# Optimization experiments

Hardware: AMD Instinct MI355X
Metric: run time of the kernel (lower is better)

## Reference

```python
import jax, jax.numpy as jnp
import numpy as np

TEMP = 0.3
K_ANCHORS = 512
SK_ITERS = 4  # max_iter=4 in the original; tol early-exit omitted (fixed small iter count)
EPS = 1e-12   # F.normalize clamp_min eps


def setup_inputs() -> dict:
    key = jax.random.key(0)
    k1, k2 = jax.random.split(key)
    x = jax.random.normal(k1, (16, 256, 64, 64), dtype=jnp.float32)
    some_idx = jax.random.randint(k2, (K_ANCHORS,), 0, 64 * 64, dtype=jnp.int32)
    return {"x": x, "some_idx": some_idx}


def sinkhorn_knopp(A):
    # A: [M, k], strictly positive. Normalize by total mass, then alternate
    # L1 column / row normalization (p=1 normalize on positive entries == sum-divide).
    A = A / A.sum()
    def body(A, _):
        A = A / jnp.clip(A.sum(axis=0, keepdims=True), EPS)  # columns
        A = A / jnp.clip(A.sum(axis=1, keepdims=True), EPS)  # rows
        return A, None
    A, _ = jax.lax.scan(body, A, None, length=SK_ITERS)
    return A


def reference(x, some_idx):
    N, C, H, W = x.shape
    k = some_idx.shape[0]
    # L2-normalize over channel dim (F.normalize dim=1)
    l2_x = x / jnp.clip(jnp.linalg.norm(x, axis=1, keepdims=True), EPS)
    # gather k random spatial anchors -> [N, C, k]
    some_x = jnp.take(l2_x.reshape(N, C, H * W), some_idx, axis=-1)
    # cosine scores [N, k, H, W]
    scores = jnp.einsum('nchw,nck->nkhw', l2_x, some_x)
    # flatten to [N*H*W, k], exponentiate, Sinkhorn-Knopp
    A = jnp.exp(scores.transpose(0, 2, 3, 1).reshape(-1, k) / TEMP)
    A = sinkhorn_knopp(A)
    Kmat = A.reshape(N, H, W, k).transpose(0, 3, 1, 2)  # [N, k, H, W]
    # reconstruct from anchors
    return jnp.einsum('nkhw,nck->nchw', Kmat, some_x)
```

## Files before the change

kernel.cpp:

```cpp
#include <hip/hip_runtime.h>
#include <hip/hip_bf16.h>
#include <hip/hip_fp16.h>
#include <hip/hip_fp8.h>

#define N_B 16
#define C_DIM 256
#define HW 4096
#define M_TOT (N_B*HW)
#define K_A 512
#define TEMP_INV (1.0f/0.3f)
#define EPS_SK 1e-12f

typedef _Float16 f16x8 __attribute__((ext_vector_type(8)));
typedef _Float16 f16x4 __attribute__((ext_vector_type(4)));
typedef float f32x4 __attribute__((ext_vector_type(4)));
typedef float f32x2 __attribute__((ext_vector_type(2)));

#if defined(__has_builtin)
#if __has_builtin(__builtin_amdgcn_cvt_pk_fp8_f32) && __has_builtin(__builtin_amdgcn_cvt_pk_f32_fp8)
#define HW_FP8 1
#endif
#endif

__device__ __forceinline__ int vperm(int j){
    return (j & ~63) | ((j & 15) << 2) | ((j & 63) >> 4);
}
__device__ __forceinline__ int ivp(int s){
    return (s & ~63) | ((s & 3) << 4) | ((s & 63) >> 2);
}

#define GLOBAL_AS __attribute__((address_space(1)))
#define LDS_AS __attribute__((address_space(3)))
__device__ __forceinline__ void gload_lds16(const void* g, void* l){
    __builtin_amdgcn_global_load_lds((GLOBAL_AS const void*)g, (LDS_AS void*)l, 16, 0, 0);
}

__device__ __forceinline__ f16x8 fp8x8_to_f16x8(uint2 a){
    f16x8 h;
#ifdef HW_FP8
    f32x2 q0 = __builtin_amdgcn_cvt_pk_f32_fp8((int)a.x, false);
    f32x2 q1 = __builtin_amdgcn_cvt_pk_f32_fp8((int)a.x, true);
    f32x2 q2 = __builtin_amdgcn_cvt_pk_f32_fp8((int)a.y, false);
    f32x2 q3 = __builtin_amdgcn_cvt_pk_f32_fp8((int)a.y, true);
    h[0]=(_Float16)q0[0]; h[1]=(_Float16)q0[1]; h[2]=(_Float16)q1[0]; h[3]=(_Float16)q1[1];
    h[4]=(_Float16)q2[0]; h[5]=(_Float16)q2[1]; h[6]=(_Float16)q3[0]; h[7]=(_Float16)q3[1];
#else
    union { uint2 u; __hip_fp8_e4m3 b8[8]; } cv; cv.u = a;
    #pragma unroll
    for (int e = 0; e < 8; ++e) h[e] = (_Float16)(float)cv.b8[e];
#endif
    return h;
}

__global__ __launch_bounds__(256) void k_normtrans(const float* __restrict__ x,
                                                   _Float16* __restrict__ Lt,
                                                   float* __restrict__ v){
    __shared__ float tl[32][257];
    __shared__ float red[8][32];
    __shared__ float invs[32];
    int n   = blockIdx.x >> 7;
    int hw0 = (blockIdx.x & 127) * 32;
    if (blockIdx.x < 2) v[blockIdx.x*256 + threadIdx.x] = 1.0f;
    int tx4 = threadIdx.x & 7;
    int cy  = threadIdx.x >> 3;
    const float* px = x + ((size_t)(n*C_DIM + cy))*HW + hw0 + tx4*4;
    #pragma unroll
    for (int r = 0; r < 8; ++r){
        float4 xv = *(const float4*)(px + (size_t)(r*32)*HW);
        int c = cy + r*32;
        tl[tx4*4+0][c] = xv.x;
        tl[tx4*4+1][c] = xv.y;
        tl[tx4*4+2][c] = xv.z;
        tl[tx4*4+3][c] = xv.w;
    }
    __syncthreads();
    int tx = threadIdx.x & 31, ty = threadIdx.x >> 5;
    float ss = 0.f;
    #pragma unroll
    for (int cc = 0; cc < 32; ++cc){
        float tv = tl[tx][cc*8 + ty];
        ss += tv*tv;
    }
    red[ty][tx] = ss;
    __syncthreads();
    if (ty == 0){
        float s = red[0][tx]+red[1][tx]+red[2][tx]+red[3][tx]
                + red[4][tx]+red[5][tx]+red[6][tx]+red[7][tx];
        invs[tx] = 1.0f / fmaxf(sqrtf(s), 1e-12f);
    }
    __syncthreads();
    #pragma unroll
    for (int r = 0; r < 4; ++r){
        int hwl = ty + r*8;
        float inv = invs[hwl];
        f16x8 h;
        #pragma unroll
        for (int e = 0; e < 8; ++e) h[e] = (_Float16)(tl[hwl][tx*8 + e] * inv);
        *(f16x8*)&Lt[((size_t)(n*HW + hw0 + hwl))*C_DIM + tx*8] = h;
    }
}

__global__ __launch_bounds__(256) void k_gather(const _Float16* __restrict__ Lt,
                                                const int* __restrict__ sidx,
                                                _Float16* __restrict__ sxT){
    int n  = blockIdx.y;
    int jj = blockIdx.x*8 + (threadIdx.x >> 5);
    int c8 = (threadIdx.x & 31) * 8;
    int p  = sidx[jj];
    *(f16x8*)&sxT[((size_t)(n*K_A + jj))*C_DIM + c8] =
        *(const f16x8*)&Lt[((size_t)(n*HW + p))*C_DIM + c8];
}

__global__ __launch_bounds__(256) void k_gemm1(const _Float16* __restrict__ Lt,
                                               const _Float16* __restrict__ sxT,
                                               unsigned* __restrict__ A8,
                                               float* __restrict__ part){
    __shared__ _Float16 As[3*128*32];
    __shared__ _Float16 Bs[3*128*32];
    __shared__ float colred[4][128];
    const int swz = (blockIdx.x & 7)*256 + (blockIdx.x >> 3);
    const int jb = swz & 3, mb = (swz >> 2) & 31, nb = swz >> 7;
    const int mbase = mb * 128;
    const int jbase = jb * 128;
    const int t = threadIdx.x;
    const int lane = t & 63, w = t >> 6;
    const int wm = (w >> 1)*64, wn = (w & 1)*64;
    const int l15 = lane & 15, lq = lane >> 4;

    f32x4 acc[4][4] = {};
    const _Float16* pa = Lt  + ((size_t)(nb*HW  + mbase))*C_DIM;
    const _Float16* pb = sxT + ((size_t)(nb*K_A + jbase))*C_DIM;

    const int r0 = t >> 2, ch = t & 3;
    const int r1 = r0 + 64;
    const int cs0 = (ch ^ ((r0 >> 1) & 3)) << 3;
    const int cs1 = (ch ^ ((r1 >> 1) & 3)) << 3;

#define STAGE1(buf, kt) { int k0 = (kt)*32; \
    gload_lds16(pa + (size_t)r0*C_DIM + k0 + cs0, &As[(buf)*4096 + t*8]); \
    gload_lds16(pa + (size_t)r1*C_DIM + k0 + cs1, &As[(buf)*4096 + (256+t)*8]); \
    gload_lds16(pb + (size_t)r0*C_DIM + k0 + cs0, &Bs[(buf)*4096 + t*8]); \
    gload_lds16(pb + (size_t)r1*C_DIM + k0 + cs1, &Bs[(buf)*4096 + (256+t)*8]); }

    STAGE1(0, 0); STAGE1(1, 1);
    #pragma unroll
    for (int kt = 0; kt < 8; ++kt){
        __builtin_amdgcn_s_barrier();
        __builtin_amdgcn_sched_barrier(0);
        if (kt < 6) STAGE1((kt+2)%3, kt+2);
        if (kt < 6)      asm volatile("s_waitcnt vmcnt(8)" ::: "memory");
        else if (kt < 7) asm volatile("s_waitcnt vmcnt(4)" ::: "memory");
        else             asm volatile("s_waitcnt vmcnt(0)" ::: "memory");
        __builtin_amdgcn_sched_barrier(0);
        const int cur = kt % 3;
        f16x8 af[4], bf[4];
        #pragma unroll
        for (int mi = 0; mi < 4; ++mi){
            int r = wm + mi*16 + l15;
            af[mi] = *(const f16x8*)&As[cur*4096 + r*32 + ((lq ^ ((r>>1)&3)) << 3)];
        }
        #pragma unroll
        for (int ni = 0; ni < 4; ++ni){
            int r = wn + ni*16 + l15;
            bf[ni] = *(const f16x8*)&Bs[cur*4096 + r*32 + ((lq ^ ((r>>1)&3)) << 3)];
        }
        #pragma unroll
        for (int mi = 0; mi < 4; ++mi)
            #pragma unroll
            for (int ni = 0; ni < 4; ++ni)
                acc[mi][ni] = __builtin_amdgcn_mfma_f32_16x16x32_f16(af[mi], bf[ni], acc[mi][ni], 0, 0, 0);
    }
    float csum[4] = {0.f, 0.f, 0.f, 0.f};
    #pragma unroll
    for (int mi = 0; mi < 4; ++mi)
        #pragma unroll
        for (int r = 0; r < 4; ++r){
            int hw = mbase + wm + mi*16 + lq*4 + r;
            float e[4];
            #pragma unroll
            for (int ni = 0; ni < 4; ++ni){
                e[ni] = __expf(acc[mi][ni][r] * TEMP_INV);
                csum[ni] += e[ni];
            }
            unsigned pk;
#ifdef HW_FP8
            pk = (unsigned)__builtin_amdgcn_cvt_pk_fp8_f32(e[0], e[1], 0, false);
            pk = (unsigned)__builtin_amdgcn_cvt_pk_fp8_f32(e[2], e[3], (int)pk, true);
#else
            union { unsigned u; __hip_fp8_e4m3 b[4]; } cv;
            cv.b[0] = __hip_fp8_e4m3(e[0]); cv.b[1] = __hip_fp8_e4m3(e[1]);
            cv.b[2] = __hip_fp8_e4m3(e[2]); cv.b[3] = __hip_fp8_e4m3(e[3]);
            pk = cv.u;
#endif
            A8[((size_t)(nb*HW + hw))*(K_A/4) + (jbase + wn)/4 + l15] = pk;
        }
    #pragma unroll
    for (int ni = 0; ni < 4; ++ni){
        float cv = csum[ni];
        cv += __shfl_xor(cv, 16);
        cv += __shfl_xor(cv, 32);
        if (lane < 16) colred[w][wn + ni*16 + l15] = cv;
    }
    __syncthreads();
    if (t < 128){
        int jj = t;
        float s = (jj < 64) ? (colred[0][jj] + colred[2][jj])
                            : (colred[1][jj] + colred[3][jj]);
        part[((size_t)(nb*32 + mb))*K_A + jbase + vperm(jj)] = s;
    }
}

__global__ __launch_bounds__(64) void k_colfinish(const float* __restrict__ part,
                                                  float* __restrict__ v, int nchunks){
    int j = blockIdx.x;
    int lane = threadIdx.x;
    float s = 0.f;
    for (int r = lane; r < nchunks; r += 64) s += part[(size_t)r*K_A + j];
    #pragma unroll
    for (int off = 32; off; off >>= 1) s += __shfl_xor(s, off);
    if (lane == 0){
        float vo = v[j];
        v[j] = 128.0f * vo / fmaxf(vo * s, EPS_SK);
    }
}

__global__ __launch_bounds__(256) void k_fused8(const unsigned* __restrict__ A8,
                                                const float* __restrict__ v,
                                                float* __restrict__ part){
    __shared__ float red[4][512];
    int b = blockIdx.x;
    int tg = threadIdx.x >> 6, lane = threadIdx.x & 63;
    float vr[8];
    const float* pv = v + (lane << 3);
    #pragma unroll
    for (int e = 0; e < 8; ++e) vr[e] = pv[e];
    float acc[8] = {};
    for (int it = 0; it < 16; ++it){
        int i = (b << 6) + (it << 2) + tg;
        uint2 a = *(const uint2*)&A8[(size_t)i*(K_A/4) + (lane << 1)];
        float av[8];
#ifdef HW_FP8
        f32x2 p0 = __builtin_amdgcn_cvt_pk_f32_fp8((int)a.x, false);
        f32x2 p1 = __builtin_amdgcn_cvt_pk_f32_fp8((int)a.x, true);
        f32x2 p2 = __builtin_amdgcn_cvt_pk_f32_fp8((int)a.y, false);
        f32x2 p3 = __builtin_amdgcn_cvt_pk_f32_fp8((int)a.y, true);
        av[0]=p0[0]; av[1]=p0[1]; av[2]=p1[0]; av[3]=p1[1];
        av[4]=p2[0]; av[5]=p2[1]; av[6]=p3[0]; av[7]=p3[1];
#else
        union { uint2 u; __hip_fp8_e4m3 b8[8]; } cv; cv.u = a;
        #pragma unroll
        for (int e = 0; e < 8; ++e) av[e] = (float)cv.b8[e];
#endif
        float r = 0.f;
        #pragma unroll
        for (int e = 0; e < 8; ++e) r += av[e] * vr[e];
        #pragma unroll
        for (int off = 32; off; off >>= 1) r += __shfl_xor(r, off);
        float un = 1.0f / fmaxf(r, EPS_SK);
        #pragma unroll
        for (int e = 0; e < 8; ++e) acc[e] += av[e] * un;
    }
    #pragma unroll
    for (int e = 0; e < 8; ++e) red[tg][(lane<<3)+e] = acc[e];
    __syncthreads();
    if (tg == 0){
        #pragma unroll
        for (int e = 0; e < 8; ++e){
            int j = (lane<<3)+e;
            part[((size_t)b)*K_A + j] = red[0][j]+red[1][j]+red[2][j]+red[3][j];
        }
    }
}

__global__ __launch_bounds__(256) void k_sxvT(const _Float16* __restrict__ sxT,
                                              const float* __restrict__ v,
                                              _Float16* __restrict__ SXv){
    __shared__ float tl[64][65];
    int n  = blockIdx.z;
    int j0 = blockIdx.x * 64;
    int c0 = blockIdx.y * 64;
    int tx = threadIdx.x & 63, ty = threadIdx.x >> 6;
    #pragma unroll
    for (int r = 0; r < 16; ++r){
        int jl = ty + r*4;
        tl[jl][tx] = (float)sxT[((size_t)(n*K_A + j0 + jl))*C_DIM + c0 + tx]
                   * v[j0 + vperm(jl)];
    }
    __syncthreads();
    #pragma unroll
    for (int r = 0; r < 16; ++r){
        int cl = ty + r*4;
        SXv[((size_t)(n*C_DIM + c0 + cl))*K_A + j0 + tx] = (_Float16)tl[ivp(tx) & 63][cl];
    }
}

__global__ __launch_bounds__(256) void k_gemm2(const _Float16* __restrict__ SXv,
                                               const unsigned* __restrict__ A8,
                                               const float* __restrict__ v,
                                               float* __restrict__ out){
    __shared__ _Float16 As[3*128*32];
    __shared__ unsigned char Bs8[3*128*32];
    __shared__ _Float16 vsh[512];
    const int swz = (blockIdx.x & 7)*128 + (blockIdx.x >> 3);
    const int mb = swz & 1, nbi = (swz >> 1) & 31, nb = swz >> 6;
    const int mbase = mb * 128;
    const int nbase = nbi * 128;
    const int t = threadIdx.x;
    const int lane = t & 63, w = t >> 6;
    const int wm = (w >> 1)*64, wn = (w & 1)*64;
    const int l15 = lane & 15, lq = lane >> 4;

    vsh[t]       = (_Float16)v[t];
    vsh[t + 256] = (_Float16)v[t + 256];

    f32x4 acc[4][4] = {};
    f32x4 racc[4] = {};
    const _Float16* pa = SXv + ((size_t)(nb*C_DIM + mbase))*K_A;
    const unsigned char* pb8 = (const unsigned char*)(A8 + ((size_t)(nb*HW + nbase))*(K_A/4));

    const int r0 = t >> 2, ch = t & 3;
    const int r1 = r0 + 64;
    const int cs0 = (ch ^ ((r0 >> 1) & 3)) << 3;
    const int cs1 = (ch ^ ((r1 >> 1) & 3)) << 3;
    const int br = t >> 1, bh = (t & 1) * 16;

#define STAGE2(buf, kt) { int k0 = (kt)*32; \
    gload_lds16(pa + (size_t)r0*K_A + k0 + cs0, &As[(buf)*4096 + t*8]); \
    gload_lds16(pa + (size_t)r1*K_A + k0 + cs1, &As[(buf)*4096 + (256+t)*8]); \
    gload_lds16(pb8 + (size_t)br*K_A + k0 + bh, &Bs8[(buf)*4096 + br*32 + bh]); }

    STAGE2(0, 0); STAGE2(1, 1);
    #pragma unroll
    for (int kt = 0; kt < 16; ++kt){
        __builtin_amdgcn_s_barrier();
        __builtin_amdgcn_sched_barrier(0);
        if (kt < 14) STAGE2((kt+2)%3, kt+2);
        if (kt < 14)      asm volatile("s_waitcnt vmcnt(6)" ::: "memory");
        else if (kt < 15) asm volatile("s_waitcnt vmcnt(3)" ::: "memory");
        else              asm volatile("s_waitcnt vmcnt(0)" ::: "memory");
        __builtin_amdgcn_sched_barrier(0);
        const int cur = kt % 3;
        f16x8 af[4], bf[4], vf;
        vf = *(const f16x8*)&vsh[kt*32 + lq*8];
        #pragma unroll
        for (int mi = 0; mi < 4; ++mi){
            int r = wm + mi*16 + l15;
            af[mi] = *(const f16x8*)&As[cur*4096 + r*32 + ((lq ^ ((r>>1)&3)) << 3)];
        }
        #pragma unroll
        for (int ni = 0; ni < 4; ++ni){
            int r = wn + ni*16 + l15;
            uint2 b8 = *(const uint2*)&Bs8[cur*4096 + r*32 + lq*8];
            bf[ni] = fp8x8_to_f16x8(b8);
        }
        #pragma unroll
        for (int mi = 0; mi < 4; ++mi)
            #pragma unroll
            for (int ni = 0; ni < 4; ++ni)
                acc[mi][ni] = __builtin_amdgcn_mfma_f32_16x16x32_f16(af[mi], bf[ni], acc[mi][ni], 0, 0, 0);
        #pragma unroll
        for (int ni = 0; ni < 4; ++ni)
            racc[ni] = __builtin_amdgcn_mfma_f32_16x16x32_f16(vf, bf[ni], racc[ni], 0, 0, 0);
    }
    float un[4];
    #pragma unroll
    for (int ni = 0; ni < 4; ++ni)
        un[ni] = 1.0f / fmaxf(racc[ni][0], EPS_SK);
    #pragma unroll
    for (int mi = 0; mi < 4; ++mi)
        #pragma unroll
        for (int ni = 0; ni < 4; ++ni)
            #pragma unroll
            for (int r = 0; r < 4; ++r){
                int c  = mbase + wm + mi*16 + lq*4 + r;
                int hw = nbase + wn + ni*16 + l15;
                out[((size_t)(nb*C_DIM + c))*HW + hw] = acc[mi][ni][r] * un[ni];
            }
}

extern "C" void kernel_launch(void* const* d_in, const int* in_sizes, int n_in,
                              void* d_out, int out_size, void* d_ws, size_t ws_size,
                              hipStream_t stream){
    const float* x  = (const float*)d_in[0];
    const int* sidx = (const int*)d_in[1];
    float* out = (float*)d_out;

    char* ws = (char*)d_ws;
    _Float16* Lt  = (_Float16*)ws;   ws += (size_t)N_B*HW*C_DIM*2;
    unsigned* A8  = (unsigned*)ws;   ws += (size_t)M_TOT*K_A;
    _Float16* sxT = (_Float16*)ws;   ws += (size_t)N_B*K_A*C_DIM*2;
    _Float16* SXv = (_Float16*)ws;   ws += (size_t)N_B*C_DIM*K_A*2;
    float*    v   = (float*)ws;      ws += (size_t)K_A*4;
    float*    part= (float*)ws;      ws += (size_t)1024*K_A*4;

    k_normtrans<<<2048, 256, 0, stream>>>(x, Lt, v);
    k_gather   <<<dim3(64,16), 256, 0, stream>>>(Lt, sidx, sxT);
    k_gemm1    <<<2048, 256, 0, stream>>>(Lt, sxT, A8, part);

    k_colfinish<<<512, 64, 0, stream>>>(part, v, 512);
    for (int it = 0; it < 3; ++it){
        k_fused8   <<<1024, 256, 0, stream>>>(A8, v, part);
        k_colfinish<<<512, 64, 0, stream>>>(part, v, 1024);
    }

    k_sxvT <<<dim3(8,4,16), 256, 0, stream>>>(sxT, v, SXv);
    k_gemm2<<<1024, 256, 0, stream>>>(SXv, A8, v, out);
}
```

Baseline: 142.9 us.

## Fold anchor gather into GEMMs and replace column-reduction kernels with atomics

Drops the separate gather kernel. gemm1 and sxvT now read anchor rows straight from the normalized tensor through sidx. Each Sinkhorn pass now atomically adds its column sums into a small per-iteration buffer instead of writing partials for a separate finish kernel, and consumers derive the scale as 128/S on the fly. This removes five kernel launches and the partial-sum traffic, and fused8 now runs with half as many blocks, each doing twice the rows. In exchange the float atomics make the sums non-deterministic, and there may be some atomic contention on 512 addresses.

```diff
diff --git a/kernel.cpp b/kernel.cpp
--- a/kernel.cpp
+++ b/kernel.cpp
@@ -54,13 +54,16 @@
 
 __global__ __launch_bounds__(256) void k_normtrans(const float* __restrict__ x,
                                                    _Float16* __restrict__ Lt,
-                                                   float* __restrict__ v){
+                                                   float* __restrict__ S){
     __shared__ float tl[32][257];
     __shared__ float red[8][32];
     __shared__ float invs[32];
     int n   = blockIdx.x >> 7;
     int hw0 = (blockIdx.x & 127) * 32;
-    if (blockIdx.x < 2) v[blockIdx.x*256 + threadIdx.x] = 1.0f;
+    if (blockIdx.x == 0){
+        #pragma unroll
+        for (int q = 0; q < 8; ++q) S[threadIdx.x + q*256] = 0.0f;
+    }
     int tx4 = threadIdx.x & 7;
     int cy  = threadIdx.x >> 3;
     const float* px = x + ((size_t)(n*C_DIM + cy))*HW + hw0 + tx4*4;
@@ -100,21 +103,10 @@
     }
 }
 
-__global__ __launch_bounds__(256) void k_gather(const _Float16* __restrict__ Lt,
-                                                const int* __restrict__ sidx,
-                                                _Float16* __restrict__ sxT){
-    int n  = blockIdx.y;
-    int jj = blockIdx.x*8 + (threadIdx.x >> 5);
-    int c8 = (threadIdx.x & 31) * 8;
-    int p  = sidx[jj];
-    *(f16x8*)&sxT[((size_t)(n*K_A + jj))*C_DIM + c8] =
-        *(const f16x8*)&Lt[((size_t)(n*HW + p))*C_DIM + c8];
-}
-
 __global__ __launch_bounds__(256) void k_gemm1(const _Float16* __restrict__ Lt,
-                                               const _Float16* __restrict__ sxT,
+                                               const int* __restrict__ sidx,
                                                unsigned* __restrict__ A8,
-                                               float* __restrict__ part){
+                                               float* __restrict__ S0){
     __shared__ _Float16 As[3*128*32];
     __shared__ _Float16 Bs[3*128*32];
     __shared__ float colred[4][128];
@@ -128,19 +120,20 @@
     const int l15 = lane & 15, lq = lane >> 4;
 
     f32x4 acc[4][4] = {};
-    const _Float16* pa = Lt  + ((size_t)(nb*HW  + mbase))*C_DIM;
-    const _Float16* pb = sxT + ((size_t)(nb*K_A + jbase))*C_DIM;
+    const _Float16* pa = Lt + ((size_t)(nb*HW + mbase))*C_DIM;
 
     const int r0 = t >> 2, ch = t & 3;
     const int r1 = r0 + 64;
     const int cs0 = (ch ^ ((r0 >> 1) & 3)) << 3;
     const int cs1 = (ch ^ ((r1 >> 1) & 3)) << 3;
+    const _Float16* pbr0 = Lt + ((size_t)(nb*HW + sidx[jbase + r0]))*C_DIM;
+    const _Float16* pbr1 = Lt + ((size_t)(nb*HW + sidx[jbase + r1]))*C_DIM;
 
 #define STAGE1(buf, kt) { int k0 = (kt)*32; \
     gload_lds16(pa + (size_t)r0*C_DIM + k0 + cs0, &As[(buf)*4096 + t*8]); \
     gload_lds16(pa + (size_t)r1*C_DIM + k0 + cs1, &As[(buf)*4096 + (256+t)*8]); \
-    gload_lds16(pb + (size_t)r0*C_DIM + k0 + cs0, &Bs[(buf)*4096 + t*8]); \
-    gload_lds16(pb + (size_t)r1*C_DIM + k0 + cs1, &Bs[(buf)*4096 + (256+t)*8]); }
+    gload_lds16(pbr0 + k0 + cs0, &Bs[(buf)*4096 + t*8]); \
+    gload_lds16(pbr1 + k0 + cs1, &Bs[(buf)*4096 + (256+t)*8]); }
 
     STAGE1(0, 0); STAGE1(1, 1);
     #pragma unroll
@@ -206,37 +199,23 @@
         int jj = t;
         float s = (jj < 64) ? (colred[0][jj] + colred[2][jj])
                             : (colred[1][jj] + colred[3][jj]);
-        part[((size_t)(nb*32 + mb))*K_A + jbase + vperm(jj)] = s;
-    }
-}
-
-__global__ __launch_bounds__(64) void k_colfinish(const float* __restrict__ part,
-                                                  float* __restrict__ v, int nchunks){
-    int j = blockIdx.x;
-    int lane = threadIdx.x;
-    float s = 0.f;
-    for (int r = lane; r < nchunks; r += 64) s += part[(size_t)r*K_A + j];
-    #pragma unroll
-    for (int off = 32; off; off >>= 1) s += __shfl_xor(s, off);
-    if (lane == 0){
-        float vo = v[j];
-        v[j] = 128.0f * vo / fmaxf(vo * s, EPS_SK);
+        atomicAdd(&S0[jbase + vperm(jj)], s);
     }
 }
 
 __global__ __launch_bounds__(256) void k_fused8(const unsigned* __restrict__ A8,
-                                                const float* __restrict__ v,
-                                                float* __restrict__ part){
+                                                const float* __restrict__ Sprev,
+                                                float* __restrict__ Snext){
     __shared__ float red[4][512];
     int b = blockIdx.x;
     int tg = threadIdx.x >> 6, lane = threadIdx.x & 63;
     float vr[8];
-    const float* pv = v + (lane << 3);
-    #pragma unroll
-    for (int e = 0; e < 8; ++e) vr[e] = pv[e];
+    const float* ps = Sprev + (lane << 3);
+    #pragma unroll
+    for (int e = 0; e < 8; ++e) vr[e] = 128.0f / fmaxf(ps[e], EPS_SK);
     float acc[8] = {};
-    for (int it = 0; it < 16; ++it){
-        int i = (b << 6) + (it << 2) + tg;
+    for (int it = 0; it < 32; ++it){
+        int i = (b << 7) + (it << 2) + tg;
         uint2 a = *(const uint2*)&A8[(size_t)i*(K_A/4) + (lane << 1)];
         float av[8];
 #ifdef HW_FP8
@@ -267,13 +246,14 @@
         #pragma unroll
         for (int e = 0; e < 8; ++e){
             int j = (lane<<3)+e;
-            part[((size_t)b)*K_A + j] = red[0][j]+red[1][j]+red[2][j]+red[3][j];
-        }
-    }
-}
-
-__global__ __launch_bounds__(256) void k_sxvT(const _Float16* __restrict__ sxT,
-                                              const float* __restrict__ v,
+            atomicAdd(&Snext[j], red[0][j]+red[1][j]+red[2][j]+red[3][j]);
+        }
+    }
+}
+
+__global__ __launch_bounds__(256) void k_sxvT(const _Float16* __restrict__ Lt,
+                                              const int* __restrict__ sidx,
+                                              const float* __restrict__ S3,
                                               _Float16* __restrict__ SXv){
     __shared__ float tl[64][65];
     int n  = blockIdx.z;
@@ -283,8 +263,9 @@
     #pragma unroll
     for (int r = 0; r < 16; ++r){
         int jl = ty + r*4;
-        tl[jl][tx] = (float)sxT[((size_t)(n*K_A + j0 + jl))*C_DIM + c0 + tx]
-                   * v[j0 + vperm(jl)];
+        float vv = 128.0f / fmaxf(S3[j0 + vperm(jl)], EPS_SK);
+        int p = sidx[j0 + jl];
+        tl[jl][tx] = (float)Lt[((size_t)(n*HW + p))*C_DIM + c0 + tx] * vv;
     }
     __syncthreads();
     #pragma unroll
@@ -296,7 +277,7 @@
 
 __global__ __launch_bounds__(256) void k_gemm2(const _Float16* __restrict__ SXv,
                                                const unsigned* __restrict__ A8,
-                                               const float* __restrict__ v,
+                                               const float* __restrict__ S3,
                                                float* __restrict__ out){
     __shared__ _Float16 As[3*128*32];
     __shared__ unsigned char Bs8[3*128*32];
@@ -310,8 +291,8 @@
     const int wm = (w >> 1)*64, wn = (w & 1)*64;
     const int l15 = lane & 15, lq = lane >> 4;
 
-    vsh[t]       = (_Float16)v[t];
-    vsh[t + 256] = (_Float16)v[t + 256];
+    vsh[t]       = (_Float16)(128.0f / fmaxf(S3[t],       EPS_SK));
+    vsh[t + 256] = (_Float16)(128.0f / fmaxf(S3[t + 256], EPS_SK));
 
     f32x4 acc[4][4] = {};
     f32x4 racc[4] = {};
@@ -388,21 +369,15 @@
     char* ws = (char*)d_ws;
     _Float16* Lt  = (_Float16*)ws;   ws += (size_t)N_B*HW*C_DIM*2;
     unsigned* A8  = (unsigned*)ws;   ws += (size_t)M_TOT*K_A;
-    _Float16* sxT = (_Float16*)ws;   ws += (size_t)N_B*K_A*C_DIM*2;
     _Float16* SXv = (_Float16*)ws;   ws += (size_t)N_B*C_DIM*K_A*2;
-    float*    v   = (float*)ws;      ws += (size_t)K_A*4;
-    float*    part= (float*)ws;      ws += (size_t)1024*K_A*4;
-
-    k_normtrans<<<2048, 256, 0, stream>>>(x, Lt, v);
-    k_gather   <<<dim3(64,16), 256, 0, stream>>>(Lt, sidx, sxT);
-    k_gemm1    <<<2048, 256, 0, stream>>>(Lt, sxT, A8, part);
-
-    k_colfinish<<<512, 64, 0, stream>>>(part, v, 512);
-    for (int it = 0; it < 3; ++it){
-        k_fused8   <<<1024, 256, 0, stream>>>(A8, v, part);
-        k_colfinish<<<512, 64, 0, stream>>>(part, v, 1024);
-    }
-
-    k_sxvT <<<dim3(8,4,16), 256, 0, stream>>>(sxT, v, SXv);
-    k_gemm2<<<1024, 256, 0, stream>>>(SXv, A8, v, out);
-}
+    float*    S   = (float*)ws;      ws += (size_t)4*K_A*4;
+
+    k_normtrans<<<2048, 256, 0, stream>>>(x, Lt, S);
+    k_gemm1    <<<2048, 256, 0, stream>>>(Lt, sidx, A8, S + 0*K_A);
+
+    for (int it = 0; it < 3; ++it)
+        k_fused8<<<512, 256, 0, stream>>>(A8, S + it*K_A, S + (it+1)*K_A);
+
+    k_sxvT <<<dim3(8,4,16), 256, 0, stream>>>(Lt, sidx, S + 3*K_A, SXv);
+    k_gemm2<<<1024, 256, 0, stream>>>(SXv, A8, S + 3*K_A, out);
+}
```

Result: slower. 415.8 us (+190.9%).
